# Performance work log

Hardware: AMD Instinct MI355X
Metric: run time of the kernel (lower is better)

## Reference

```python
import jax, jax.numpy as jnp
import numpy as np

# MaskingConfig constants
NUM_BLOCKS = 4          # config.num_target_blocks
SCALE_MIN = 0.15        # config.target_scale_min
SCALE_MAX = 0.2         # config.target_scale_max

BATCH = 256
SEQ_LEN = 131072


def setup_inputs() -> dict:
    key = jax.random.key(0)
    k1, k2 = jax.random.split(key)
    total_spans = BATCH * NUM_BLOCKS
    # uniform draws underlying torch's .uniform_() and torch.rand()
    scales_u = jax.random.uniform(k1, (total_spans,), dtype=jnp.float32)
    starts_u = jax.random.uniform(k2, (total_spans,), dtype=jnp.float32)
    return {"scales_u": scales_u, "starts_u": starts_u,
            "batch_size": BATCH, "seq_len": SEQ_LEN}


def reference(scales_u, starts_u, batch_size, seq_len):
    # scales ~ U(SCALE_MIN, SCALE_MAX)
    scales = SCALE_MIN + scales_u * (SCALE_MAX - SCALE_MIN)
    # span_lens = clamp(int(scales * seq_len), min=1); .int() truncates (positive -> floor)
    span_lens = jnp.maximum((scales * seq_len).astype(jnp.int32), 1)          # [T]
    max_starts = jnp.maximum(seq_len - span_lens, 0)                          # [T]
    # starts = int(rand * (max_starts + 1))
    starts = (starts_u * (max_starts.astype(jnp.float32) + 1.0)).astype(jnp.int32)
    ends = jnp.minimum(starts + span_lens, seq_len)                           # [T]

    pos = jnp.arange(seq_len, dtype=jnp.int32)                                # [S]
    # span coverage via broadcasted comparison: [T, S] bool
    cover = (pos[None, :] >= starts[:, None]) & (pos[None, :] < ends[:, None])
    # OR the num_blocks spans belonging to each batch item
    target_mask = cover.reshape(batch_size, NUM_BLOCKS, seq_len).any(axis=1)  # [B, S]
    context_mask = ~target_mask

    # padded replacement for the ragged per-batch nonzero list:
    # masked positions first (ascending), padded with seq_len sentinel
    padded_positions = jnp.sort(
        jnp.where(target_mask, pos[None, :], seq_len), axis=1)                # [B, S] int32
    return context_mask, target_mask, padded_positions
```

## Files before the change

kernel.cpp:

```cpp
#include <hip/hip_runtime.h>


constexpr int S_LEN = 131072;
constexpr int NBLK  = 4;
constexpr int TPB   = 256;
constexpr int ITEMS = 16;

typedef int int4v __attribute__((ext_vector_type(4)));

__global__ __launch_bounds__(TPB) void span_mask_kernel(
    const float* __restrict__ scales_u,
    const float* __restrict__ starts_u,
    int* __restrict__ out,
    int batch)
{
    const int b = blockIdx.y;

    int ss[NBLK], ee[NBLK];
#pragma unroll
    for (int t = 0; t < NBLK; ++t) {
        float u  = scales_u[b * NBLK + t];
        float r  = starts_u[b * NBLK + t];
        float sc = __fadd_rn(0.15f, __fmul_rn(u, 0.05f));
        int len  = (int)__fmul_rn(sc, 131072.0f);
        if (len < 1) len = 1;
        int mx   = S_LEN - len; if (mx < 0) mx = 0;
        int st   = (int)__fmul_rn(r, __fadd_rn((float)mx, 1.0f));
        int en   = st + len; if (en > S_LEN) en = S_LEN;
        ss[t] = st; ee[t] = en;
    }

#define CSWAP(i, j)                                                        \
    if (ss[i] > ss[j]) {                                                   \
        int t0 = ss[i]; ss[i] = ss[j]; ss[j] = t0;                         \
        int t1 = ee[i]; ee[i] = ee[j]; ee[j] = t1;                         \
    }
    CSWAP(0, 1) CSWAP(2, 3) CSWAP(0, 2) CSWAP(1, 3) CSWAP(1, 2)
#undef CSWAP

    const int L0 = ss[0],          R0 = ee[0];
    const int L1 = max(ss[1], R0), R1 = max(ee[1], R0);
    const int L2 = max(ss[2], R1), R2 = max(ee[2], R1);
    const int L3 = max(ss[3], R2), R3 = max(ee[3], R2);
    const int c1 = R0 - L0;
    const int c2 = c1 + (R1 - L1);
    const int c3 = c2 + (R2 - L2);
    const int total = c3 + (R3 - L3);

    const size_t BS   = (size_t)batch * S_LEN;
    const size_t base = (size_t)b * S_LEN;
    int* __restrict__ ctx = out + base;
    int* __restrict__ tgt = out + BS + base;
    int* __restrict__ pad = out + 2 * BS + base;

    const int blockStart = blockIdx.x * (TPB * ITEMS);

#pragma unroll
    for (int q = 0; q < ITEMS / 4; ++q) {
        const int s0 = blockStart + q * (TPB * 4) + threadIdx.x * 4;
        int cv[4], tv[4], pv[4];
#pragma unroll
        for (int j = 0; j < 4; ++j) {
            const int s = s0 + j;
            const int cov =
                ((s >= ss[0]) & (s < ee[0])) | ((s >= ss[1]) & (s < ee[1])) |
                ((s >= ss[2]) & (s < ee[2])) | ((s >= ss[3]) & (s < ee[3]));
            tv[j] = cov;
            cv[j] = cov ^ 1;
            int v;
            if      (s >= total) v = S_LEN;
            else if (s >= c3)    v = L3 + (s - c3);
            else if (s >= c2)    v = L2 + (s - c2);
            else if (s >= c1)    v = L1 + (s - c1);
            else                 v = L0 + s;
            pv[j] = v;
        }
        int4v c4 = { cv[0], cv[1], cv[2], cv[3] };
        int4v t4 = { tv[0], tv[1], tv[2], tv[3] };
        int4v p4 = { pv[0], pv[1], pv[2], pv[3] };
        *(reinterpret_cast<int4v*>(ctx + s0)) = c4;
        *(reinterpret_cast<int4v*>(tgt + s0)) = t4;
        *(reinterpret_cast<int4v*>(pad + s0)) = p4;
    }
}

extern "C" void kernel_launch(void* const* d_in, const int* in_sizes, int n_in,
                              void* d_out, int out_size, void* d_ws, size_t ws_size,
                              hipStream_t stream)
{
    const float* scales_u = (const float*)d_in[0];
    const float* starts_u = (const float*)d_in[1];
    const int batch = 256;
    dim3 grid(S_LEN / (TPB * ITEMS), batch);
    span_mask_kernel<<<grid, dim3(TPB), 0, stream>>>(
        scales_u, starts_u, (int*)d_out, batch);
}
```

Before: 78.75 us.

## Split the three output tensors across grid z so each block writes one stream

Adds a third grid dimension so each block writes only one of the context, target or padded-position outputs, instead of all three interleaved. It also doubles items per thread so the total block count stays at one and a half times the original. The goal is to make each block's stores contiguous in one region and to cut per-thread work and register use. In exchange, every block now recomputes the span bounds, and the branch on the z index adds a little control flow.

```diff
diff --git a/kernel.cpp b/kernel.cpp
--- a/kernel.cpp
+++ b/kernel.cpp
@@ -4,7 +4,7 @@
 constexpr int S_LEN = 131072;
 constexpr int NBLK  = 4;
 constexpr int TPB   = 256;
-constexpr int ITEMS = 16;
+constexpr int ITEMS = 32;
 
 typedef int int4v __attribute__((ext_vector_type(4)));
 
@@ -14,7 +14,8 @@
     int* __restrict__ out,
     int batch)
 {
-    const int b = blockIdx.y;
+    const int b     = blockIdx.y;
+    const int which = blockIdx.z;
 
     int ss[NBLK], ee[NBLK];
 #pragma unroll
@@ -47,40 +48,47 @@
     const int c3 = c2 + (R2 - L2);
     const int total = c3 + (R3 - L3);
 
-    const size_t BS   = (size_t)batch * S_LEN;
-    const size_t base = (size_t)b * S_LEN;
-    int* __restrict__ ctx = out + base;
-    int* __restrict__ tgt = out + BS + base;
-    int* __restrict__ pad = out + 2 * BS + base;
+    const size_t BS = (size_t)batch * S_LEN;
+    int* __restrict__ dst = out + (size_t)which * BS + (size_t)b * S_LEN;
 
     const int blockStart = blockIdx.x * (TPB * ITEMS);
 
+    if (which < 2) {
+        const int flip = which ^ 1;
 #pragma unroll
-    for (int q = 0; q < ITEMS / 4; ++q) {
-        const int s0 = blockStart + q * (TPB * 4) + threadIdx.x * 4;
-        int cv[4], tv[4], pv[4];
+        for (int q = 0; q < ITEMS / 4; ++q) {
+            const int s0 = blockStart + q * (TPB * 4) + threadIdx.x * 4;
+            int v[4];
 #pragma unroll
-        for (int j = 0; j < 4; ++j) {
-            const int s = s0 + j;
-            const int cov =
-                ((s >= ss[0]) & (s < ee[0])) | ((s >= ss[1]) & (s < ee[1])) |
-                ((s >= ss[2]) & (s < ee[2])) | ((s >= ss[3]) & (s < ee[3]));
-            tv[j] = cov;
-            cv[j] = cov ^ 1;
-            int v;
-            if      (s >= total) v = S_LEN;
-            else if (s >= c3)    v = L3 + (s - c3);
-            else if (s >= c2)    v = L2 + (s - c2);
-            else if (s >= c1)    v = L1 + (s - c1);
-            else                 v = L0 + s;
-            pv[j] = v;
+            for (int j = 0; j < 4; ++j) {
+                const int s = s0 + j;
+                const int cov =
+                    ((s >= ss[0]) & (s < ee[0])) | ((s >= ss[1]) & (s < ee[1])) |
+                    ((s >= ss[2]) & (s < ee[2])) | ((s >= ss[3]) & (s < ee[3]));
+                v[j] = cov ^ flip;
+            }
+            int4v v4 = { v[0], v[1], v[2], v[3] };
+            *(reinterpret_cast<int4v*>(dst + s0)) = v4;
         }
-        int4v c4 = { cv[0], cv[1], cv[2], cv[3] };
-        int4v t4 = { tv[0], tv[1], tv[2], tv[3] };
-        int4v p4 = { pv[0], pv[1], pv[2], pv[3] };
-        *(reinterpret_cast<int4v*>(ctx + s0)) = c4;
-        *(reinterpret_cast<int4v*>(tgt + s0)) = t4;
-        *(reinterpret_cast<int4v*>(pad + s0)) = p4;
+    } else {
+#pragma unroll
+        for (int q = 0; q < ITEMS / 4; ++q) {
+            const int s0 = blockStart + q * (TPB * 4) + threadIdx.x * 4;
+            int v[4];
+#pragma unroll
+            for (int j = 0; j < 4; ++j) {
+                const int s = s0 + j;
+                int p;
+                if      (s >= total) p = S_LEN;
+                else if (s >= c3)    p = L3 + (s - c3);
+                else if (s >= c2)    p = L2 + (s - c2);
+                else if (s >= c1)    p = L1 + (s - c1);
+                else                 p = L0 + s;
+                v[j] = p;
+            }
+            int4v v4 = { v[0], v[1], v[2], v[3] };
+            *(reinterpret_cast<int4v*>(dst + s0)) = v4;
+        }
     }
 }
 
@@ -91,7 +99,7 @@
     const float* scales_u = (const float*)d_in[0];
     const float* starts_u = (const float*)d_in[1];
     const int batch = 256;
-    dim3 grid(S_LEN / (TPB * ITEMS), batch);
+    dim3 grid(S_LEN / (TPB * ITEMS), batch, 3);
     span_mask_kernel<<<grid, dim3(TPB), 0, stream>>>(
         scales_u, starts_u, (int*)d_out, batch);
 }
```

Result: no change. 79.54 us (+1.0%).
